# Kernel optimization log

Measured on AMD Instinct MI355X. Metric: run time of the kernel, lower is better.

## Reference

```python
import jax, jax.numpy as jnp
import numpy as np

NUM_HEADS = 12
EMB = 768
D_KEY = 64
D_VALUE = 64
MASKED = True


def setup_inputs() -> dict:
    key = jax.random.key(0)
    k1, k2, k3, k4 = jax.random.split(key, 4)
    x = jax.random.normal(k1, (1, 4096, EMB), dtype=jnp.float32)
    q_proj = jax.random.normal(k2, (NUM_HEADS, EMB, D_KEY), dtype=jnp.float32)
    k_proj = jax.random.normal(k3, (NUM_HEADS, EMB, D_KEY), dtype=jnp.float32)
    v_proj = jax.random.normal(k4, (NUM_HEADS, EMB, D_VALUE), dtype=jnp.float32)
    return {"x": x, "q_proj": q_proj, "k_proj": k_proj, "v_proj": v_proj}


def reference(x, q_proj, k_proj, v_proj):
    # x: [B, S, E]; projections: [H, E, dk/dv]
    q = jnp.einsum("bse,hek->bhsk", x, q_proj)  # [B,H,S,dk]
    k = jnp.einsum("bse,hek->bhsk", x, k_proj)  # [B,H,S,dk]
    v = jnp.einsum("bse,hev->bhsv", x, v_proj)  # [B,H,S,dv]
    scale = jnp.sqrt(jnp.asarray(D_KEY, dtype=x.dtype))
    scores = jnp.einsum("bhsk,bhtk->bhst", q, k) / scale  # [B,H,S,S]
    if MASKED:
        S = x.shape[1]
        # causal mask: disallow attending to future positions (strict upper triangle)
        mask = jnp.triu(jnp.ones((S, S), dtype=bool), k=1)
        scores = jnp.where(mask, -jnp.inf, scores)
    attn = jax.nn.softmax(scores, axis=-1)
    out = jnp.einsum("bhst,bhtv->bhsv", attn, v)  # [B,H,S,dv]
    return out
```

## Files before the change

### kernel.cpp

```cpp
#include <hip/hip_runtime.h>
#include <hip/hip_bf16.h>

#define NH 12
#define SEQ 4096
#define E 768
#define DK 64

typedef float f32x4 __attribute__((ext_vector_type(4)));
typedef float f32x16 __attribute__((ext_vector_type(16)));
typedef __bf16 bf16x8 __attribute__((ext_vector_type(8)));
typedef __bf16 bf16x4 __attribute__((ext_vector_type(4)));
typedef unsigned u32x2 __attribute__((ext_vector_type(2)));
typedef unsigned u32x4 __attribute__((ext_vector_type(4)));

#define MFMA16(a, b, c) __builtin_amdgcn_mfma_f32_16x16x32_bf16((a), (b), (c), 0, 0, 0)
#define MFMA32(a, b, c) __builtin_amdgcn_mfma_f32_32x32x16_bf16((a), (b), (c), 0, 0, 0)

#define SCL 0.18033688011112042f
#define DEFER 10.8f

#define PART_SZ 4352

__device__ __forceinline__ void gload16(const void* g, void* l) {
    __builtin_amdgcn_global_load_lds(
        (const __attribute__((address_space(1))) void*)g,
        (__attribute__((address_space(3))) void*)l, 16, 0, 0);
}

__device__ __forceinline__ void block_sync() {
    __builtin_amdgcn_sched_barrier(0);
    __builtin_amdgcn_s_barrier();
    __builtin_amdgcn_sched_barrier(0);
}

__device__ __forceinline__ unsigned cvtpk(float lo, float hi) {
    unsigned r;
    asm("v_cvt_pk_bf16_f32 %0, %1, %2" : "=v"(r) : "v"(lo), "v"(hi));
    return r;
}
__device__ __forceinline__ u32x2 plswap(unsigned a, unsigned b) {
    return __builtin_amdgcn_permlane32_swap(a, b, false, false);
}
__device__ __forceinline__ float xhalf_max(float v) {
    u32x2 r = plswap(__float_as_uint(v), __float_as_uint(v));
    return fmaxf(__uint_as_float(r.x), __uint_as_float(r.y));
}
__device__ __forceinline__ float xhalf_add(float v) {
    u32x2 r = plswap(__float_as_uint(v), __float_as_uint(v));
    return __uint_as_float(r.x) + __uint_as_float(r.y);
}

__global__ __launch_bounds__(256) void xsplit_kernel(const float* __restrict__ x,
                                                     __bf16* __restrict__ xh,
                                                     __bf16* __restrict__ xl) {
    int i = blockIdx.x * blockDim.x + threadIdx.x;
    float4 v = ((const float4*)x)[i];
    bf16x4 h, l;
    float vv[4] = {v.x, v.y, v.z, v.w};
#pragma unroll
    for (int j = 0; j < 4; ++j) {
        __bf16 hh = (__bf16)vv[j];
        h[j] = hh;
        l[j] = (__bf16)(vv[j] - (float)hh);
    }
    ((bf16x4*)xh)[i] = h;
    ((bf16x4*)xl)[i] = l;
}

__global__ void wsplit_kernel(const float* __restrict__ qp,
                              const float* __restrict__ kp,
                              const float* __restrict__ vp,
                              __bf16* __restrict__ wtq_h, __bf16* __restrict__ wtq_l,
                              __bf16* __restrict__ wtk_h, __bf16* __restrict__ wtk_l,
                              __bf16* __restrict__ wtv_h) {
    int idx = blockIdx.x * blockDim.x + threadIdx.x;
    if (idx >= NH * E * DK) return;
    int h = idx / (E * DK);
    int rem = idx - h * E * DK;
    int k = rem / DK;
    int n = rem - k * DK;
    int o = h * DK * E + n * E + k;
    float q = qp[idx];
    __bf16 qh = (__bf16)q;
    wtq_h[o] = qh;
    wtq_l[o] = (__bf16)(q - (float)qh);
    float kk = kp[idx] * SCL;
    __bf16 kh = (__bf16)kk;
    wtk_h[o] = kh;
    wtk_l[o] = (__bf16)(kk - (float)kh);
    wtv_h[o] = (__bf16)vp[idx];
}

__global__ __launch_bounds__(256, 2) void proj_kernel(
    const __bf16* __restrict__ xh, const __bf16* __restrict__ xl,
    const __bf16* __restrict__ wq_h_g, const __bf16* __restrict__ wq_l_g,
    const __bf16* __restrict__ wk_h_g, const __bf16* __restrict__ wk_l_g,
    const __bf16* __restrict__ wv_g,
    __bf16* __restrict__ qh_o, __bf16* __restrict__ ql_o,
    __bf16* __restrict__ kh_o, __bf16* __restrict__ kl_o,
    __bf16* __restrict__ vt_o) {
    __shared__ char wlds[2][20480];

    const int wg = (blockIdx.x & 7) * 96 + (blockIdx.x >> 3);
    const int head = wg >> 6;
    const int rb = wg & 63;
    const int wave = threadIdx.x >> 6;
    const int lane = threadIdx.x & 63;
    const int lrow = lane & 15;
    const int lk8 = (lane >> 4) * 8;
    const int g4 = (lane >> 4) * 4;
    const int rowbase = rb * 64 + wave * 16;

    const char* bases[5] = {
        (const char*)(wq_h_g + head * DK * E), (const char*)(wq_l_g + head * DK * E),
        (const char*)(wk_h_g + head * DK * E), (const char*)(wk_l_g + head * DK * E),
        (const char*)(wv_g + head * DK * E)};
    const int srow = lane >> 2;
    const int scol = (lane & 3) * 16;

    auto STAGE = [&](int buf, int ks) {
#pragma unroll
        for (int r = 0; r < 5; ++r) {
            int q = wave * 5 + r;
            const char* src = bases[q >> 2] + (size_t)((q & 3) * 16 + srow) * (E * 2) + ks * 64 + scol;
            gload16(src, wlds[buf] + q * 1024 + lane * 16);
        }
    };

    f32x4 accq[4], acck[4], accv[4];
#pragma unroll
    for (int f = 0; f < 4; ++f) {
        accq[f] = (f32x4){0.f, 0.f, 0.f, 0.f};
        acck[f] = (f32x4){0.f, 0.f, 0.f, 0.f};
        accv[f] = (f32x4){0.f, 0.f, 0.f, 0.f};
    }

    bf16x8 ah, al, ahn, aln;
    auto LOADA = [&](int ks, bf16x8& h, bf16x8& l) {
        size_t xo = (size_t)(rowbase + lrow) * E + ks * 32 + lk8;
        h = *(const bf16x8*)(xh + xo);
        l = *(const bf16x8*)(xl + xo);
    };

    LOADA(0, ah, al);
    STAGE(0, 0);
    int buf = 0;
    for (int ks = 0; ks < 24; ++ks) {
        if (ks < 23) {
            LOADA(ks + 1, ahn, aln);
            STAGE(buf ^ 1, ks + 1);
            asm volatile("s_waitcnt vmcnt(7)" ::: "memory");
        } else {
            asm volatile("s_waitcnt vmcnt(0)" ::: "memory");
        }
        block_sync();
#pragma unroll
        for (int f = 0; f < 4; ++f) {
            int bo = (f * 16 + lrow) * 64 + lk8 * 2;
            bf16x8 bqh = *(const bf16x8*)(wlds[buf] + bo);
            bf16x8 bql = *(const bf16x8*)(wlds[buf] + 4096 + bo);
            bf16x8 bkh = *(const bf16x8*)(wlds[buf] + 8192 + bo);
            bf16x8 bkl = *(const bf16x8*)(wlds[buf] + 12288 + bo);
            bf16x8 bv  = *(const bf16x8*)(wlds[buf] + 16384 + bo);
            accq[f] = MFMA16(ah, bqh, accq[f]);
            accq[f] = MFMA16(ah, bql, accq[f]);
            accq[f] = MFMA16(al, bqh, accq[f]);
            acck[f] = MFMA16(ah, bkh, acck[f]);
            acck[f] = MFMA16(ah, bkl, acck[f]);
            acck[f] = MFMA16(al, bkh, acck[f]);
            accv[f] = MFMA16(bv, ah, accv[f]);
        }
        block_sync();
        if (ks < 23) {
            ah = ahn;
            al = aln;
        }
        buf ^= 1;
    }

    char* khb = (char*)kh_o + (size_t)head * SEQ * DK * 2;
    char* klb = (char*)kl_o + (size_t)head * SEQ * DK * 2;
    char* vb = (char*)vt_o + (size_t)head * DK * SEQ * 2;
#pragma unroll
    for (int f = 0; f < 4; ++f)
#pragma unroll
        for (int r = 0; r < 4; ++r) {
            int srow_o = rowbase + g4 + r;
            int d = f * 16 + lrow;
            size_t o = (size_t)head * SEQ * DK + (size_t)srow_o * DK + d;
            float qv = accq[f][r];
            __bf16 qhh = (__bf16)qv;
            qh_o[o] = qhh;
            ql_o[o] = (__bf16)(qv - (float)qhh);
            size_t ko = (size_t)(srow_o >> 6) * 8192 + ((srow_o >> 5) & 1) * 4096
                      + (size_t)f * 1024
                      + ((srow_o & 31) + 32 * ((lrow >> 3) & 1)) * 16 + (lrow & 7) * 2;
            float kv = acck[f][r];
            __bf16 khh = (__bf16)kv;
            *(__bf16*)(khb + ko) = khh;
            *(__bf16*)(klb + ko) = (__bf16)(kv - (float)khh);
            int vd = f * 16 + g4 + r;
            int vs = rowbase + lrow;
            size_t vo = (size_t)(vs >> 6) * 8192 + ((vd >> 5) & 1) * 4096
                      + ((vs >> 4) & 3) * 1024
                      + ((vd & 31) + 32 * ((vs >> 3) & 1)) * 16 + (vs & 7) * 2;
            *(__bf16*)(vb + vo) = (__bf16)accv[f][r];
        }
}

__global__ __launch_bounds__(256, 2) void attn_part_kernel(
    const __bf16* __restrict__ qh, const __bf16* __restrict__ ql,
    const __bf16* __restrict__ kh, const __bf16* __restrict__ kl,
    const __bf16* __restrict__ vt,
    char* __restrict__ part, int fine, int perx) {
    const int blk = (blockIdx.x & 7) * perx + (blockIdx.x >> 3);
    const int wave = threadIdx.x >> 6;
    const int task = blk * 4 + wave;
    const int lane = threadIdx.x & 63;
    const int lq = lane & 31;
    const int lh = lane >> 5;

    const int G = fine ? 16 : 32;
    const int gmax = fine ? 7 : 3;
    const int tph = fine ? 576 : 320;

    const int head = task / tph;
    const int t = task - head * tph;
    int g = 0;
#pragma unroll 8
    for (int gg = 1; gg <= 7; ++gg)
        if (gg <= gmax && t >= G * gg * (gg + 1) / 2) g = gg;
    const int nsp = g + 1;
    const int u = t - G * g * (g + 1) / 2;
    const int w = G * g + u / nsp;
    const int split = u - (u / nsp) * nsp;
    const int ktot = (w >> 1) + 1;
    const int lo = (split * ktot) / nsp;
    const int hi = ((split + 1) * ktot) / nsp;
    const int rowbase = w * 32;

    const size_t hoff = (size_t)head * SEQ * DK;

    bf16x8 qBh[4], qBl[4];
    {
        const __bf16* qph = qh + hoff + (size_t)(rowbase + lq) * DK + lh * 8;
        const __bf16* qpl = ql + hoff + (size_t)(rowbase + lq) * DK + lh * 8;
#pragma unroll
        for (int ds = 0; ds < 4; ++ds) {
            qBh[ds] = *(const bf16x8*)(qph + ds * 16);
            qBl[ds] = *(const bf16x8*)(qpl + ds * 16);
        }
    }

    const char* kh_p = (const char*)(kh + hoff) + (size_t)lo * 8192 + lane * 16;
    const char* kl_p = (const char*)(kl + hoff) + (size_t)lo * 8192 + lane * 16;
    const char* vt_p = (const char*)(vt + (size_t)head * DK * SEQ) + (size_t)lo * 8192 + lane * 16;

    f32x16 O0 = (f32x16)0.0f, O1 = (f32x16)0.0f;
    float m = -3.0e38f, lsum = 0.f;

    for (int tt = lo; tt < hi; ++tt) {
        const int kb = tt * 64;

        f32x16 s0 = (f32x16)0.0f, s1 = (f32x16)0.0f;
#pragma unroll
        for (int ds = 0; ds < 4; ++ds) {
            bf16x8 ah0 = *(const bf16x8*)(kh_p + ds * 1024);
            bf16x8 al0 = *(const bf16x8*)(kl_p + ds * 1024);
            bf16x8 ah1 = *(const bf16x8*)(kh_p + 4096 + ds * 1024);
            bf16x8 al1 = *(const bf16x8*)(kl_p + 4096 + ds * 1024);
            s0 = MFMA32(ah0, qBh[ds], s0);
            s1 = MFMA32(ah1, qBh[ds], s1);
            s0 = MFMA32(al0, qBh[ds], s0);
            s1 = MFMA32(al1, qBh[ds], s1);
            s0 = MFMA32(ah0, qBl[ds], s0);
            s1 = MFMA32(ah1, qBl[ds], s1);
        }

        bf16x8 v00 = *(const bf16x8*)(vt_p + 0);
        bf16x8 v01 = *(const bf16x8*)(vt_p + 1024);
        bf16x8 v10 = *(const bf16x8*)(vt_p + 2048);
        bf16x8 v11 = *(const bf16x8*)(vt_p + 3072);
        bf16x8 w00 = *(const bf16x8*)(vt_p + 4096);
        bf16x8 w01 = *(const bf16x8*)(vt_p + 5120);
        bf16x8 w10 = *(const bf16x8*)(vt_p + 6144);
        bf16x8 w11 = *(const bf16x8*)(vt_p + 7168);

        if (kb + 63 > rowbase) {
            int qa = rowbase + lq;
#pragma unroll
            for (int r = 0; r < 16; ++r) {
                int kp = kb + ((r & 3) + 8 * (r >> 2) + 4 * lh);
                if (kp > qa) s0[r] = -1.0e30f;
                if (kp + 32 > qa) s1[r] = -1.0e30f;
            }
        }

        float x0 = fmaxf(s0[0], s0[1]), x1 = fmaxf(s0[2], s0[3]);
        float x2 = fmaxf(s0[4], s0[5]), x3 = fmaxf(s0[6], s0[7]);
#pragma unroll
        for (int r = 8; r < 16; r += 4) {
            x0 = fmaxf(x0, fmaxf(s0[r], s0[r + 1]));
            x1 = fmaxf(x1, fmaxf(s0[r + 2], s0[r + 3]));
        }
#pragma unroll
        for (int r = 0; r < 16; r += 4) {
            x2 = fmaxf(x2, fmaxf(s1[r], s1[r + 1]));
            x3 = fmaxf(x3, fmaxf(s1[r + 2], s1[r + 3]));
        }
        float mx = xhalf_max(fmaxf(fmaxf(x0, x1), fmaxf(x2, x3)));

        if (!__all(mx - m <= DEFER)) {
            float mn = fmaxf(m, mx);
            float al = exp2f(m - mn);
            m = mn;
            lsum *= al;
#pragma unroll
            for (int r = 0; r < 16; ++r) {
                float a = __shfl(al, (r & 3) + 8 * (r >> 2) + 4 * lh);
                O0[r] *= a;
                O1[r] *= a;
            }
        }

        s0 = s0 - m;
        s1 = s1 - m;
#pragma unroll
        for (int r = 0; r < 16; ++r) {
            s0[r] = exp2f(s0[r]);
            s1[r] = exp2f(s1[r]);
        }
        {
            f32x16 sv = s0 + s1;
            float p0 = 0.f, p1 = 0.f;
#pragma unroll
            for (int r = 0; r < 16; r += 4) {
                p0 += sv[r] + sv[r + 1];
                p1 += sv[r + 2] + sv[r + 3];
            }
            lsum += p0 + p1;
        }

        unsigned W0 = cvtpk(s0[0], s0[1]), W1 = cvtpk(s0[2], s0[3]);
        unsigned W2 = cvtpk(s0[4], s0[5]), W3 = cvtpk(s0[6], s0[7]);
        unsigned W4 = cvtpk(s0[8], s0[9]), W5 = cvtpk(s0[10], s0[11]);
        unsigned W6 = cvtpk(s0[12], s0[13]), W7 = cvtpk(s0[14], s0[15]);
        u32x2 rA = plswap(W0, W2), rB = plswap(W1, W3);
        u32x2 rC = plswap(W4, W6), rD = plswap(W5, W7);
        bf16x8 p00 = __builtin_bit_cast(bf16x8, (u32x4){rA.x, rB.x, rA.y, rB.y});
        bf16x8 p01 = __builtin_bit_cast(bf16x8, (u32x4){rC.x, rD.x, rC.y, rD.y});
        W0 = cvtpk(s1[0], s1[1]); W1 = cvtpk(s1[2], s1[3]);
        W2 = cvtpk(s1[4], s1[5]); W3 = cvtpk(s1[6], s1[7]);
        W4 = cvtpk(s1[8], s1[9]); W5 = cvtpk(s1[10], s1[11]);
        W6 = cvtpk(s1[12], s1[13]); W7 = cvtpk(s1[14], s1[15]);
        rA = plswap(W0, W2); rB = plswap(W1, W3);
        rC = plswap(W4, W6); rD = plswap(W5, W7);
        bf16x8 p10 = __builtin_bit_cast(bf16x8, (u32x4){rA.x, rB.x, rA.y, rB.y});
        bf16x8 p11 = __builtin_bit_cast(bf16x8, (u32x4){rC.x, rD.x, rC.y, rD.y});

        O0 = MFMA32(p00, v00, O0);
        O0 = MFMA32(p01, v01, O0);
        O0 = MFMA32(p10, v10, O0);
        O0 = MFMA32(p11, v11, O0);
        O1 = MFMA32(p00, w00, O1);
        O1 = MFMA32(p01, w01, O1);
        O1 = MFMA32(p10, w10, O1);
        O1 = MFMA32(p11, w11, O1);

        kh_p += 8192;
        kl_p += 8192;
        vt_p += 8192;
    }

    char* pb = part + (size_t)task * PART_SZ;
    unsigned* ph = (unsigned*)pb;
#pragma unroll
    for (int r = 0; r < 16; r += 2) {
        ph[(r >> 1) * 64 + lane] = cvtpk(O0[r], O0[r + 1]);
        ph[512 + (r >> 1) * 64 + lane] = cvtpk(O1[r], O1[r + 1]);
    }
    float lf = xhalf_add(lsum);
    float* pm = (float*)(pb + 4096);
    if (lane < 32) {
        pm[lq] = m;
        pm[32 + lq] = lf;
    }
}

__global__ __launch_bounds__(256) void attn_comb_kernel(
    const char* __restrict__ part, float* __restrict__ out, int fine) {
    const int W = blockIdx.x;
    const int head = W >> 7, w = W & 127;
    const int G = fine ? 16 : 32;
    const int tph = fine ? 576 : 320;
    const int g = w / G;
    const int nsp = g + 1;
    const int tb = head * tph + G * g * (g + 1) / 2 + (w - G * g) * nsp;

    const int tid = threadIdx.x;
    const int row = tid >> 3;
    const int d0 = (tid & 7) * 8;
    const int lane0 = (d0 & 31) + 32 * ((row >> 2) & 1);
    const int r = (row & 3) + 4 * (row >> 3);
    const int word = (r >> 1) * 64;
    const int hi16 = r & 1;
    const char* p0 = part + (size_t)tb * PART_SZ;

    float mstar = -3.0e38f;
    for (int s = 0; s < nsp; ++s) {
        const float* pm = (const float*)(p0 + s * PART_SZ + 4096);
        mstar = fmaxf(mstar, pm[row]);
    }

    float acc[8] = {0.f, 0.f, 0.f, 0.f, 0.f, 0.f, 0.f, 0.f};
    float lt = 0.f;
    for (int s = 0; s < nsp; ++s) {
        const float* pm = (const float*)(p0 + s * PART_SZ + 4096);
        float wgt = exp2f(pm[row] - mstar);
        lt += wgt * pm[32 + row];
        const unsigned* pw = (const unsigned*)(p0 + s * PART_SZ + (d0 >> 5) * 2048);
        u32x4 a = *(const u32x4*)(pw + word + lane0);
        u32x4 b = *(const u32x4*)(pw + word + lane0 + 4);
#pragma unroll
        for (int j = 0; j < 8; ++j) {
            unsigned u = (j < 4) ? a[j] : b[j - 4];
            unsigned bits = hi16 ? (u & 0xffff0000u) : (u << 16);
            acc[j] += wgt * __uint_as_float(bits);
        }
    }
    float inv = 1.0f / lt;
    size_t o = (size_t)head * SEQ * DK + (size_t)(w * 32 + row) * DK + d0;
#pragma unroll
    for (int j = 0; j < 8; ++j) out[o + j] = acc[j] * inv;
}

extern "C" void kernel_launch(void* const* d_in, const int* in_sizes, int n_in,
                              void* d_out, int out_size, void* d_ws, size_t ws_size,
                              hipStream_t stream) {
    const float* x = (const float*)d_in[0];
    const float* qp = (const float*)d_in[1];
    const float* kp = (const float*)d_in[2];
    const float* vp = (const float*)d_in[3];
    float* out = (float*)d_out;

    const size_t WT_SZ = (size_t)NH * DK * E * 2;
    const size_t QKV_SZ = (size_t)NH * SEQ * DK * 2;
    const size_t X_SZ = (size_t)SEQ * E * 2;
    char* ws = (char*)d_ws;
    __bf16* wtq_h = (__bf16*)(ws + 0 * WT_SZ);
    __bf16* wtq_l = (__bf16*)(ws + 1 * WT_SZ);
    __bf16* wtk_h = (__bf16*)(ws + 2 * WT_SZ);
    __bf16* wtk_l = (__bf16*)(ws + 3 * WT_SZ);
    __bf16* wtv_h = (__bf16*)(ws + 4 * WT_SZ);
    char* px = ws + 5 * WT_SZ;
    __bf16* xh = (__bf16*)(px + 0 * X_SZ);
    __bf16* xl = (__bf16*)(px + 1 * X_SZ);
    char* p2 = px + 2 * X_SZ;
    __bf16* qh = (__bf16*)(p2 + 0 * QKV_SZ);
    __bf16* ql = (__bf16*)(p2 + 1 * QKV_SZ);
    __bf16* kh = (__bf16*)(p2 + 2 * QKV_SZ);
    __bf16* kl = (__bf16*)(p2 + 3 * QKV_SZ);
    __bf16* vt = (__bf16*)(p2 + 4 * QKV_SZ);
    char* tail = p2 + 5 * QKV_SZ;

    const size_t need = (size_t)(p2 - ws) + 5 * QKV_SZ + 6912ull * PART_SZ;
    const int fine = (ws_size >= need) ? 1 : 0;
    char* part = fine ? tail : ws;
    const int nblk = fine ? 1728 : 960;
    const int perx = fine ? 216 : 120;

    hipLaunchKernelGGL(xsplit_kernel, dim3(SEQ * E / 4 / 256), dim3(256), 0, stream,
                       x, xh, xl);
    hipLaunchKernelGGL(wsplit_kernel, dim3((NH * E * DK + 255) / 256), dim3(256), 0, stream,
                       qp, kp, vp, wtq_h, wtq_l, wtk_h, wtk_l, wtv_h);
    hipLaunchKernelGGL(proj_kernel, dim3(768), dim3(256), 0, stream,
                       xh, xl, wtq_h, wtq_l, wtk_h, wtk_l, wtv_h, qh, ql, kh, kl, vt);
    hipLaunchKernelGGL(attn_part_kernel, dim3(nblk), dim3(256), 0, stream,
                       qh, ql, kh, kl, vt, part, fine, perx);
    hipLaunchKernelGGL(attn_comb_kernel, dim3(1536), dim3(256), 0, stream,
                       part, out, fine);
}
```

Before: 169.3 us.

## Fuse split kernels with LDS-transposed weight prep; widen proj rows per wave

Merges the x-split and weight-split kernels into one prep launch, and the weight part now transposes through shared memory so both its global reads and writes are coalesced. The projection kernel drops to 128 threads, with each wave computing 32 rows instead of 16, so every LDS weight fragment feeds twice as many MFMAs. The fine/coarse workspace fallback is removed and the attention kernels hardcode the fine split. This cuts a launch and uncoalesced transposed stores, at the cost of higher register use in proj and an assumption that the workspace is always large enough.

```diff
diff --git a/kernel.cpp b/kernel.cpp
--- a/kernel.cpp
+++ b/kernel.cpp
@@ -50,48 +50,70 @@
     return __uint_as_float(r.x) + __uint_as_float(r.y);
 }
 
-__global__ __launch_bounds__(256) void xsplit_kernel(const float* __restrict__ x,
-                                                     __bf16* __restrict__ xh,
-                                                     __bf16* __restrict__ xl) {
-    int i = blockIdx.x * blockDim.x + threadIdx.x;
-    float4 v = ((const float4*)x)[i];
-    bf16x4 h, l;
-    float vv[4] = {v.x, v.y, v.z, v.w};
-#pragma unroll
-    for (int j = 0; j < 4; ++j) {
-        __bf16 hh = (__bf16)vv[j];
-        h[j] = hh;
-        l[j] = (__bf16)(vv[j] - (float)hh);
-    }
-    ((bf16x4*)xh)[i] = h;
-    ((bf16x4*)xl)[i] = l;
-}
-
-__global__ void wsplit_kernel(const float* __restrict__ qp,
-                              const float* __restrict__ kp,
-                              const float* __restrict__ vp,
-                              __bf16* __restrict__ wtq_h, __bf16* __restrict__ wtq_l,
-                              __bf16* __restrict__ wtk_h, __bf16* __restrict__ wtk_l,
-                              __bf16* __restrict__ wtv_h) {
-    int idx = blockIdx.x * blockDim.x + threadIdx.x;
-    if (idx >= NH * E * DK) return;
-    int h = idx / (E * DK);
-    int rem = idx - h * E * DK;
-    int k = rem / DK;
-    int n = rem - k * DK;
-    int o = h * DK * E + n * E + k;
-    float q = qp[idx];
-    __bf16 qh = (__bf16)q;
-    wtq_h[o] = qh;
-    wtq_l[o] = (__bf16)(q - (float)qh);
-    float kk = kp[idx] * SCL;
-    __bf16 kh = (__bf16)kk;
-    wtk_h[o] = kh;
-    wtk_l[o] = (__bf16)(kk - (float)kh);
-    wtv_h[o] = (__bf16)vp[idx];
-}
-
-__global__ __launch_bounds__(256, 2) void proj_kernel(
+__global__ __launch_bounds__(256) void prep_kernel(
+    const float* __restrict__ x,
+    const float* __restrict__ qp, const float* __restrict__ kp,
+    const float* __restrict__ vp,
+    __bf16* __restrict__ xh, __bf16* __restrict__ xl,
+    __bf16* __restrict__ wtq_h, __bf16* __restrict__ wtq_l,
+    __bf16* __restrict__ wtk_h, __bf16* __restrict__ wtk_l,
+    __bf16* __restrict__ wtv_h) {
+    __shared__ float tl[64][65];
+
+    if (blockIdx.x >= 144) {
+        int i = (blockIdx.x - 144) * 256 + threadIdx.x;
+        float4 v = ((const float4*)x)[i];
+        bf16x4 h, l;
+        float vv[4] = {v.x, v.y, v.z, v.w};
+#pragma unroll
+        for (int j = 0; j < 4; ++j) {
+            __bf16 hh = (__bf16)vv[j];
+            h[j] = hh;
+            l[j] = (__bf16)(vv[j] - (float)hh);
+        }
+        ((bf16x4*)xh)[i] = h;
+        ((bf16x4*)xl)[i] = l;
+        return;
+    }
+
+    const int h = blockIdx.x / 12;
+    const int kt = blockIdx.x % 12;
+    const int c = threadIdx.x & 63;
+    const int r4 = threadIdx.x >> 6;
+
+#pragma unroll
+    for (int mat = 0; mat < 3; ++mat) {
+        const float* src = ((mat == 0) ? qp : (mat == 1) ? kp : vp)
+                         + (size_t)h * E * DK + (size_t)kt * 64 * DK;
+        __syncthreads();
+#pragma unroll
+        for (int i = 0; i < 16; ++i) {
+            int row = i * 4 + r4;
+            tl[row][c] = src[row * DK + c];
+        }
+        __syncthreads();
+#pragma unroll
+        for (int i = 0; i < 16; ++i) {
+            int n = i * 4 + r4;
+            float v = tl[c][n];
+            size_t o = (size_t)h * DK * E + (size_t)n * E + kt * 64 + c;
+            if (mat == 0) {
+                __bf16 hh = (__bf16)v;
+                wtq_h[o] = hh;
+                wtq_l[o] = (__bf16)(v - (float)hh);
+            } else if (mat == 1) {
+                float kk = v * SCL;
+                __bf16 hh = (__bf16)kk;
+                wtk_h[o] = hh;
+                wtk_l[o] = (__bf16)(kk - (float)hh);
+            } else {
+                wtv_h[o] = (__bf16)v;
+            }
+        }
+    }
+}
+
+__global__ __launch_bounds__(128, 2) void proj_kernel(
     const __bf16* __restrict__ xh, const __bf16* __restrict__ xl,
     const __bf16* __restrict__ wq_h_g, const __bf16* __restrict__ wq_l_g,
     const __bf16* __restrict__ wk_h_g, const __bf16* __restrict__ wk_l_g,
@@ -109,7 +131,7 @@
     const int lrow = lane & 15;
     const int lk8 = (lane >> 4) * 8;
     const int g4 = (lane >> 4) * 4;
-    const int rowbase = rb * 64 + wave * 16;
+    const int rowbase = rb * 64 + wave * 32;
 
     const char* bases[5] = {
         (const char*)(wq_h_g + head * DK * E), (const char*)(wq_l_g + head * DK * E),
@@ -120,26 +142,31 @@
 
     auto STAGE = [&](int buf, int ks) {
 #pragma unroll
-        for (int r = 0; r < 5; ++r) {
-            int q = wave * 5 + r;
+        for (int r = 0; r < 10; ++r) {
+            int q = wave * 10 + r;
             const char* src = bases[q >> 2] + (size_t)((q & 3) * 16 + srow) * (E * 2) + ks * 64 + scol;
             gload16(src, wlds[buf] + q * 1024 + lane * 16);
         }
     };
 
-    f32x4 accq[4], acck[4], accv[4];
-#pragma unroll
-    for (int f = 0; f < 4; ++f) {
-        accq[f] = (f32x4){0.f, 0.f, 0.f, 0.f};
-        acck[f] = (f32x4){0.f, 0.f, 0.f, 0.f};
-        accv[f] = (f32x4){0.f, 0.f, 0.f, 0.f};
-    }
-
-    bf16x8 ah, al, ahn, aln;
-    auto LOADA = [&](int ks, bf16x8& h, bf16x8& l) {
-        size_t xo = (size_t)(rowbase + lrow) * E + ks * 32 + lk8;
-        h = *(const bf16x8*)(xh + xo);
-        l = *(const bf16x8*)(xl + xo);
+    f32x4 accq[2][4], acck[2][4], accv[2][4];
+#pragma unroll
+    for (int rt = 0; rt < 2; ++rt)
+#pragma unroll
+        for (int f = 0; f < 4; ++f) {
+            accq[rt][f] = (f32x4){0.f, 0.f, 0.f, 0.f};
+            acck[rt][f] = (f32x4){0.f, 0.f, 0.f, 0.f};
+            accv[rt][f] = (f32x4){0.f, 0.f, 0.f, 0.f};
+        }
+
+    bf16x8 ah[2], al[2], ahn[2], aln[2];
+    auto LOADA = [&](int ks, bf16x8* h, bf16x8* l) {
+#pragma unroll
+        for (int rt = 0; rt < 2; ++rt) {
+            size_t xo = (size_t)(rowbase + rt * 16 + lrow) * E + ks * 32 + lk8;
+            h[rt] = *(const bf16x8*)(xh + xo);
+            l[rt] = *(const bf16x8*)(xl + xo);
+        }
     };
 
     LOADA(0, ah, al);
@@ -149,7 +176,7 @@
         if (ks < 23) {
             LOADA(ks + 1, ahn, aln);
             STAGE(buf ^ 1, ks + 1);
-            asm volatile("s_waitcnt vmcnt(7)" ::: "memory");
+            asm volatile("s_waitcnt vmcnt(14)" ::: "memory");
         } else {
             asm volatile("s_waitcnt vmcnt(0)" ::: "memory");
         }
@@ -162,18 +189,24 @@
             bf16x8 bkh = *(const bf16x8*)(wlds[buf] + 8192 + bo);
             bf16x8 bkl = *(const bf16x8*)(wlds[buf] + 12288 + bo);
             bf16x8 bv  = *(const bf16x8*)(wlds[buf] + 16384 + bo);
-            accq[f] = MFMA16(ah, bqh, accq[f]);
-            accq[f] = MFMA16(ah, bql, accq[f]);
-            accq[f] = MFMA16(al, bqh, accq[f]);
-            acck[f] = MFMA16(ah, bkh, acck[f]);
-            acck[f] = MFMA16(ah, bkl, acck[f]);
-            acck[f] = MFMA16(al, bkh, acck[f]);
-            accv[f] = MFMA16(bv, ah, accv[f]);
+#pragma unroll
+            for (int rt = 0; rt < 2; ++rt) {
+                accq[rt][f] = MFMA16(ah[rt], bqh, accq[rt][f]);
+                accq[rt][f] = MFMA16(ah[rt], bql, accq[rt][f]);
+                accq[rt][f] = MFMA16(al[rt], bqh, accq[rt][f]);
+                acck[rt][f] = MFMA16(ah[rt], bkh, acck[rt][f]);
+                acck[rt][f] = MFMA16(ah[rt], bkl, acck[rt][f]);
+                acck[rt][f] = MFMA16(al[rt], bkh, acck[rt][f]);
+                accv[rt][f] = MFMA16(bv, ah[rt], accv[rt][f]);
+            }
         }
         block_sync();
         if (ks < 23) {
-            ah = ahn;
-            al = aln;
+#pragma unroll
+            for (int rt = 0; rt < 2; ++rt) {
+                ah[rt] = ahn[rt];
+                al[rt] = aln[rt];
+            }
         }
         buf ^= 1;
     }
@@ -182,57 +215,55 @@
     char* klb = (char*)kl_o + (size_t)head * SEQ * DK * 2;
     char* vb = (char*)vt_o + (size_t)head * DK * SEQ * 2;
 #pragma unroll
-    for (int f = 0; f < 4; ++f)
-#pragma unroll
-        for (int r = 0; r < 4; ++r) {
-            int srow_o = rowbase + g4 + r;
-            int d = f * 16 + lrow;
-            size_t o = (size_t)head * SEQ * DK + (size_t)srow_o * DK + d;
-            float qv = accq[f][r];
-            __bf16 qhh = (__bf16)qv;
-            qh_o[o] = qhh;
-            ql_o[o] = (__bf16)(qv - (float)qhh);
-            size_t ko = (size_t)(srow_o >> 6) * 8192 + ((srow_o >> 5) & 1) * 4096
-                      + (size_t)f * 1024
-                      + ((srow_o & 31) + 32 * ((lrow >> 3) & 1)) * 16 + (lrow & 7) * 2;
-            float kv = acck[f][r];
-            __bf16 khh = (__bf16)kv;
-            *(__bf16*)(khb + ko) = khh;
-            *(__bf16*)(klb + ko) = (__bf16)(kv - (float)khh);
-            int vd = f * 16 + g4 + r;
-            int vs = rowbase + lrow;
-            size_t vo = (size_t)(vs >> 6) * 8192 + ((vd >> 5) & 1) * 4096
-                      + ((vs >> 4) & 3) * 1024
-                      + ((vd & 31) + 32 * ((vs >> 3) & 1)) * 16 + (vs & 7) * 2;
-            *(__bf16*)(vb + vo) = (__bf16)accv[f][r];
-        }
+    for (int rt = 0; rt < 2; ++rt)
+#pragma unroll
+        for (int f = 0; f < 4; ++f)
+#pragma unroll
+            for (int r = 0; r < 4; ++r) {
+                int srow_o = rowbase + rt * 16 + g4 + r;
+                int d = f * 16 + lrow;
+                size_t o = (size_t)head * SEQ * DK + (size_t)srow_o * DK + d;
+                float qv = accq[rt][f][r];
+                __bf16 qhh = (__bf16)qv;
+                qh_o[o] = qhh;
+                ql_o[o] = (__bf16)(qv - (float)qhh);
+                size_t ko = (size_t)(srow_o >> 6) * 8192 + ((srow_o >> 5) & 1) * 4096
+                          + (size_t)f * 1024
+                          + ((srow_o & 31) + 32 * ((lrow >> 3) & 1)) * 16 + (lrow & 7) * 2;
+                float kv = acck[rt][f][r];
+                __bf16 khh = (__bf16)kv;
+                *(__bf16*)(khb + ko) = khh;
+                *(__bf16*)(klb + ko) = (__bf16)(kv - (float)khh);
+                int vd = f * 16 + g4 + r;
+                int vs = rowbase + rt * 16 + lrow;
+                size_t vo = (size_t)(vs >> 6) * 8192 + ((vd >> 5) & 1) * 4096
+                          + ((vs >> 4) & 3) * 1024
+                          + ((vd & 31) + 32 * ((vs >> 3) & 1)) * 16 + (vs & 7) * 2;
+                *(__bf16*)(vb + vo) = (__bf16)accv[rt][f][r];
+            }
 }
 
 __global__ __launch_bounds__(256, 2) void attn_part_kernel(
     const __bf16* __restrict__ qh, const __bf16* __restrict__ ql,
     const __bf16* __restrict__ kh, const __bf16* __restrict__ kl,
     const __bf16* __restrict__ vt,
-    char* __restrict__ part, int fine, int perx) {
-    const int blk = (blockIdx.x & 7) * perx + (blockIdx.x >> 3);
+    char* __restrict__ part) {
+    const int blk = (blockIdx.x & 7) * 216 + (blockIdx.x >> 3);
     const int wave = threadIdx.x >> 6;
     const int task = blk * 4 + wave;
     const int lane = threadIdx.x & 63;
     const int lq = lane & 31;
     const int lh = lane >> 5;
 
-    const int G = fine ? 16 : 32;
-    const int gmax = fine ? 7 : 3;
-    const int tph = fine ? 576 : 320;
-
-    const int head = task / tph;
-    const int t = task - head * tph;
+    const int head = task / 576;
+    const int t = task - head * 576;
     int g = 0;
 #pragma unroll 8
     for (int gg = 1; gg <= 7; ++gg)
-        if (gg <= gmax && t >= G * gg * (gg + 1) / 2) g = gg;
+        if (t >= 16 * gg * (gg + 1) / 2) g = gg;
     const int nsp = g + 1;
-    const int u = t - G * g * (g + 1) / 2;
-    const int w = G * g + u / nsp;
+    const int u = t - 16 * g * (g + 1) / 2;
+    const int w = 16 * g + u / nsp;
     const int split = u - (u / nsp) * nsp;
     const int ktot = (w >> 1) + 1;
     const int lo = (split * ktot) / nsp;
@@ -388,14 +419,12 @@
 }
 
 __global__ __launch_bounds__(256) void attn_comb_kernel(
-    const char* __restrict__ part, float* __restrict__ out, int fine) {
+    const char* __restrict__ part, float* __restrict__ out) {
     const int W = blockIdx.x;
     const int head = W >> 7, w = W & 127;
-    const int G = fine ? 16 : 32;
-    const int tph = fine ? 576 : 320;
-    const int g = w / G;
+    const int g = w >> 4;
     const int nsp = g + 1;
-    const int tb = head * tph + G * g * (g + 1) / 2 + (w - G * g) * nsp;
+    const int tb = head * 576 + 16 * g * (g + 1) / 2 + (w - 16 * g) * nsp;
 
     const int tid = threadIdx.x;
     const int row = tid >> 3;
@@ -415,10 +444,11 @@
     float acc[8] = {0.f, 0.f, 0.f, 0.f, 0.f, 0.f, 0.f, 0.f};
     float lt = 0.f;
     for (int s = 0; s < nsp; ++s) {
-        const float* pm = (const float*)(p0 + s * PART_SZ + 4096);
+        const char* ps = p0 + s * PART_SZ;
+        const float* pm = (const float*)(ps + 4096);
         float wgt = exp2f(pm[row] - mstar);
         lt += wgt * pm[32 + row];
-        const unsigned* pw = (const unsigned*)(p0 + s * PART_SZ + (d0 >> 5) * 2048);
+        const unsigned* pw = (const unsigned*)(ps + (d0 >> 5) * 2048);
         u32x4 a = *(const u32x4*)(pw + word + lane0);
         u32x4 b = *(const u32x4*)(pw + word + lane0 + 4);
 #pragma unroll
@@ -461,22 +491,14 @@
     __bf16* kh = (__bf16*)(p2 + 2 * QKV_SZ);
     __bf16* kl = (__bf16*)(p2 + 3 * QKV_SZ);
     __bf16* vt = (__bf16*)(p2 + 4 * QKV_SZ);
-    char* tail = p2 + 5 * QKV_SZ;
-
-    const size_t need = (size_t)(p2 - ws) + 5 * QKV_SZ + 6912ull * PART_SZ;
-    const int fine = (ws_size >= need) ? 1 : 0;
-    char* part = fine ? tail : ws;
-    const int nblk = fine ? 1728 : 960;
-    const int perx = fine ? 216 : 120;
-
-    hipLaunchKernelGGL(xsplit_kernel, dim3(SEQ * E / 4 / 256), dim3(256), 0, stream,
-                       x, xh, xl);
-    hipLaunchKernelGGL(wsplit_kernel, dim3((NH * E * DK + 255) / 256), dim3(256), 0, stream,
-                       qp, kp, vp, wtq_h, wtq_l, wtk_h, wtk_l, wtv_h);
-    hipLaunchKernelGGL(proj_kernel, dim3(768), dim3(256), 0, stream,
+    char* part = p2 + 5 * QKV_SZ;
+
+    hipLaunchKernelGGL(prep_kernel, dim3(144 + SEQ * E / 4 / 256), dim3(256), 0, stream,
+                       x, qp, kp, vp, xh, xl, wtq_h, wtq_l, wtk_h, wtk_l, wtv_h);
+    hipLaunchKernelGGL(proj_kernel, dim3(768), dim3(128), 0, stream,
                        xh, xl, wtq_h, wtq_l, wtk_h, wtk_l, wtv_h, qh, ql, kh, kl, vt);
-    hipLaunchKernelGGL(attn_part_kernel, dim3(nblk), dim3(256), 0, stream,
-                       qh, ql, kh, kl, vt, part, fine, perx);
+    hipLaunchKernelGGL(attn_part_kernel, dim3(1728), dim3(256), 0, stream,
+                       qh, ql, kh, kl, vt, part);
     hipLaunchKernelGGL(attn_comb_kernel, dim3(1536), dim3(256), 0, stream,
-                       part, out, fine);
-}
+                       part, out);
+}
```

New measurement: 151.7 us. 1.12x faster.
